# Kernel tuning notes

Hardware: AMD Instinct MI355X
Metric: run time of the kernel (lower is better)

Reference implementation:

```python
import jax, jax.numpy as jnp
import numpy as np

B, T, N, C_IN, C_OUT, CHEB_K, ST_EMB = 8, 12, 2048, 64, 64, 2, 64


def setup_inputs() -> dict:
    key = jax.random.key(0)
    ks = jax.random.split(key, 9)
    inv = 1.0 / np.sqrt(ST_EMB)
    return {
        "x": jax.random.normal(ks[0], (B, T, N, C_IN), dtype=jnp.float32),
        "adj": jax.random.uniform(ks[1], (N, N), dtype=jnp.float32),
        "st_emb": jax.random.normal(ks[2], (T, 1, ST_EMB), dtype=jnp.float32),
        "weights": jax.random.normal(ks[3], (CHEB_K, C_IN, C_OUT), dtype=jnp.float32) * 0.02,
        "bias": jax.random.normal(ks[4], (C_OUT,), dtype=jnp.float32) * 0.02,
        "W1": jax.random.uniform(ks[5], (ST_EMB, 32), minval=-inv, maxval=inv, dtype=jnp.float32),
        "b1": jax.random.uniform(ks[6], (32,), minval=-inv, maxval=inv, dtype=jnp.float32),
        "W2": jax.random.uniform(ks[7], (32, 1), minval=-1/np.sqrt(32), maxval=1/np.sqrt(32), dtype=jnp.float32),
        "b2": jax.random.uniform(ks[8], (1,), minval=-1/np.sqrt(32), maxval=1/np.sqrt(32), dtype=jnp.float32),
    }


def reference(x, adj, st_emb, weights, bias, W1, b1, W2, b2):
    # lambda MLP: Linear -> ReLU -> Linear, then 1 + relu(.)
    h = jax.nn.relu(st_emb @ W1 + b1)            # [T,1,32]
    lam = 1.0 + jax.nn.relu(h @ W2 + b2)         # [T,1,1]
    c1 = (2.0 * lam - 2.0) / lam                 # [T,1,1] diagonal-scale coefficient
    c2 = 2.0 / lam                               # [T,1,1]
    # identity support einsum == per-time diagonal scaling of x
    x_g1 = c1[None] * x                          # [B,T,N,C]
    # adjacency support: scale factored out of the N x N contraction
    x_g2 = c2[None] * jnp.einsum('nm,btmc->btnc', adj, x)  # [B,T,N,C]
    x_g = jnp.stack([x_g1, x_g2], axis=3)        # [B,T,N,K,C]
    return jnp.einsum('btnki,kio->btno', x_g, weights) + bias
```

## Files before the change

### kernel.cpp

```cpp
#include <hip/hip_runtime.h>
#include <hip/hip_bf16.h>

#define B_ 8
#define T_ 12
#define N_ 2048
#define C_ 64
#define BM 128
#define BK 64

typedef __attribute__((ext_vector_type(4))) float f32x4;
typedef __attribute__((ext_vector_type(4))) __bf16 bf16x4;
typedef __attribute__((ext_vector_type(8))) __bf16 bf16x8;

#define GAS __attribute__((address_space(1)))
#define LAS __attribute__((address_space(3)))

static __device__ __forceinline__ void gld_lds16(const void* g, void* l) {
    __builtin_amdgcn_global_load_lds((const GAS void*)g, (LAS void*)l, 16, 0, 0);
}

#define WS_CBUF 0
#define WS_WTB  1024
#define WS_ADJB 32768
#define WS_P1T  (32768 + 8388608)
#define WS_P0S  (WS_P1T + 25165824)
#define WS_MID  ((size_t)WS_P0S)
#define WS_FULL ((size_t)WS_P0S + 25165824)

__global__ void lam_kernel(const float* __restrict__ st, const float* __restrict__ W1,
                           const float* __restrict__ b1, const float* __restrict__ W2,
                           const float* __restrict__ b2, float* __restrict__ cbuf) {
    const int t = threadIdx.x >> 5;
    const int h = threadIdx.x & 31;
    if (t >= T_) return;
    float acc = b1[h];
    #pragma unroll 8
    for (int e = 0; e < 64; ++e) acc += st[t * 64 + e] * W1[e * 32 + h];
    float hv = fmaxf(acc, 0.f) * W2[h];
    #pragma unroll
    for (int off = 16; off; off >>= 1) hv += __shfl_down(hv, off, 32);
    if (h == 0) {
        float lam = 1.f + fmaxf(hv + b2[0], 0.f);
        cbuf[t]      = 2.f - 2.f / lam;
        cbuf[T_ + t] = 2.f / lam;
    }
}

__global__ void lamw_kernel(const float* __restrict__ st, const float* __restrict__ W1,
                            const float* __restrict__ b1, const float* __restrict__ W2,
                            const float* __restrict__ b2, const float* __restrict__ weights,
                            float* __restrict__ cbuf, __bf16* __restrict__ WtB) {
    const int t = threadIdx.x >> 5;
    const int h = threadIdx.x & 31;
    if (t < T_) {
        float acc = b1[h];
        #pragma unroll 8
        for (int e = 0; e < 64; ++e) acc += st[t * 64 + e] * W1[e * 32 + h];
        float hv = fmaxf(acc, 0.f) * W2[h];
        #pragma unroll
        for (int off = 16; off; off >>= 1) hv += __shfl_down(hv, off, 32);
        if (h == 0) {
            float lam = 1.f + fmaxf(hv + b2[0], 0.f);
            cbuf[t]      = 2.f - 2.f / lam;
            cbuf[T_ + t] = 2.f / lam;
        }
    }
    for (int e = threadIdx.x; e < 64 * 128; e += 512) {
        int o = e >> 7, k = e & 127;
        float v = (k < 64) ? weights[4096 + k * 64 + o] : weights[(k - 64) * 64 + o];
        WtB[o * 128 + k] = (__bf16)v;
    }
}

template<bool FULLP>
__global__ __launch_bounds__(256, 4) void pcvt_kernel(
    const float* __restrict__ x, const float* __restrict__ adj,
    const __bf16* __restrict__ WtB, const float* __restrict__ cbuf,
    const float* __restrict__ bias, __bf16* __restrict__ adjb,
    __bf16* __restrict__ P1T, __bf16* __restrict__ P0S, float* __restrict__ out)
{
    const int bid = blockIdx.x;
    const int tid = threadIdx.x;
    if (bid >= 1536) {
        const size_t i = ((size_t)(bid - 1536) * 256 + tid) * 8;
        const float4 f0 = *(const float4*)&adj[i];
        const float4 f1 = *(const float4*)&adj[i + 4];
        bf16x8 h = { (__bf16)f0.x, (__bf16)f0.y, (__bf16)f0.z, (__bf16)f0.w,
                     (__bf16)f1.x, (__bf16)f1.y, (__bf16)f1.z, (__bf16)f1.w };
        *(bf16x8*)&adjb[i] = h;
        return;
    }
    __shared__ __align__(16) __bf16 T[64 * 128];
    char* TB = (char*)T;
    const int bt = bid >> 4, n0 = (bid & 15) * 128;
    const int l = tid & 63, w = tid >> 6;
    const int lr = l & 15, lk = l >> 4;
    const float c1 = cbuf[bt % T_];

    f32x4 p1[2][4] = {}, p0[2][4] = {};
    #pragma unroll
    for (int ks = 0; ks < 2; ++ks) {
        bf16x8 a[2];
        #pragma unroll
        for (int mi = 0; mi < 2; ++mi) {
            const float* xs = x + ((size_t)bt * N_ + n0 + w * 32 + mi * 16 + lr) * C_ + ks * 32 + lk * 8;
            float4 f0 = *(const float4*)xs;
            float4 f1 = *(const float4*)(xs + 4);
            a[mi] = { (__bf16)f0.x, (__bf16)f0.y, (__bf16)f0.z, (__bf16)f0.w,
                      (__bf16)f1.x, (__bf16)f1.y, (__bf16)f1.z, (__bf16)f1.w };
        }
        #pragma unroll
        for (int nj = 0; nj < 4; ++nj) {
            const __bf16* wb = WtB + (nj * 16 + lr) * 128 + ks * 32 + lk * 8;
            bf16x8 b1v = *(const bf16x8*)wb;
            bf16x8 b0v = *(const bf16x8*)(wb + 64);
            #pragma unroll
            for (int mi = 0; mi < 2; ++mi) {
                p1[mi][nj] = __builtin_amdgcn_mfma_f32_16x16x32_bf16(a[mi], b1v, p1[mi][nj], 0, 0, 0);
                p0[mi][nj] = __builtin_amdgcn_mfma_f32_16x16x32_bf16(a[mi], b0v, p0[mi][nj], 0, 0, 0);
            }
        }
    }
    #pragma unroll
    for (int nj = 0; nj < 4; ++nj) {
        const int o = nj * 16 + lr;
        const float bv = bias[o];
        #pragma unroll
        for (int mi = 0; mi < 2; ++mi)
            #pragma unroll
            for (int q = 0; q < 4; ++q) {
                const int row = w * 32 + mi * 16 + lk * 4 + q;
                const size_t idx = ((size_t)bt * N_ + n0 + row) * C_ + o;
                const float v = c1 * p0[mi][nj][q] + bv;
                if (FULLP) P0S[idx] = (__bf16)v; else out[idx] = v;
            }
    }
    #pragma unroll
    for (int nj = 0; nj < 4; ++nj) {
        const int o = nj * 16 + lr;
        #pragma unroll
        for (int mi = 0; mi < 2; ++mi)
            #pragma unroll
            for (int q = 0; q < 4; ++q) {
                const int row = w * 32 + mi * 16 + lk * 4 + q;
                *(__bf16*)(TB + o * 256 + ((row * 2) ^ ((o & 7) << 4))) = (__bf16)p1[mi][nj][q];
            }
    }
    __syncthreads();
    {
        const int o = tid >> 2, seg = tid & 3;
        __bf16* dst = P1T + ((size_t)bt * 64 + o) * N_ + n0 + seg * 32;
        #pragma unroll
        for (int i = 0; i < 4; ++i) {
            const int chunk = seg * 64 + i * 16;
            *(bf16x8*)(dst + i * 8) = *(const bf16x8*)(TB + o * 256 + (chunk ^ ((o & 7) << 4)));
        }
    }
}

template<bool FULLP>
__global__ __launch_bounds__(256, 2) void dgcn_main3(
    const __bf16* __restrict__ adjb, const __bf16* __restrict__ P1T,
    const __bf16* __restrict__ P0S, const float* __restrict__ cbuf,
    float* __restrict__ out)
{
    __shared__ __align__(16) __bf16 smem[40960];
    char* sb = (char*)smem;

    const int m0  = blockIdx.x * BM;
    const int btg = blockIdx.y;
    const int tid = threadIdx.x;
    const int l   = tid & 63, w = tid >> 6;
    const int wr  = w >> 1, wc = w & 1;
    const int lr  = l & 15, lk = l >> 4;

    const __bf16* srcA[4];
    const __bf16* srcB[6];
    #pragma unroll
    for (int i = 0; i < 4; ++i) {
        int s = (w * 4 + i) * 64 + l;
        int r = s >> 3, j = s & 7;
        srcA[i] = adjb + (size_t)(m0 + r) * N_ + 8 * (j ^ (r & 7));
    }
    #pragma unroll
    for (int i = 0; i < 6; ++i) {
        int s = (w * 6 + i) * 64 + l;
        int btl = s >> 9, rem = s & 511;
        int o = rem >> 3, j = rem & 7;
        srcB[i] = P1T + ((size_t)(btg * 3 + btl) * 64 + o) * N_ + 8 * (j ^ (o & 7));
    }

    f32x4 acc[4][6] = {};

    #pragma unroll
    for (int i = 0; i < 4; ++i) gld_lds16(srcA[i], sb + (w * 4 + i) * 1024);
    #pragma unroll
    for (int i = 0; i < 6; ++i) gld_lds16(srcB[i], sb + 16384 + (w * 6 + i) * 1024);

    int sel = 0;
    for (int kt = 0; kt < N_ / BK; ++kt) {
        __syncthreads();
        if (kt < N_ / BK - 1) {
            const int wo = (sel ^ 1) * 40960;
            #pragma unroll
            for (int i = 0; i < 4; ++i) {
                srcA[i] += BK;
                gld_lds16(srcA[i], sb + wo + (w * 4 + i) * 1024);
            }
            #pragma unroll
            for (int i = 0; i < 6; ++i) {
                srcB[i] += BK;
                gld_lds16(srcB[i], sb + wo + 16384 + (w * 6 + i) * 1024);
            }
        }
        const char* base = sb + sel * 40960;
        #pragma unroll
        for (int ks = 0; ks < 2; ++ks) {
            const int kb = ks * 64 + lk * 16;
            bf16x8 a[4];
            #pragma unroll
            for (int mi = 0; mi < 4; ++mi) {
                int rr = wr * 64 + mi * 16 + lr;
                a[mi] = *(const bf16x8*)(base + rr * 128 + (kb ^ ((rr & 7) << 4)));
            }
            #pragma unroll
            for (int nj = 0; nj < 6; ++nj) {
                int c = wc * 96 + nj * 16 + lr;
                int btl = c >> 6, o = c & 63;
                bf16x8 b = *(const bf16x8*)(base + 16384 + btl * 8192 + o * 128 + (kb ^ ((o & 7) << 4)));
                #pragma unroll
                for (int mi = 0; mi < 4; ++mi)
                    acc[mi][nj] = __builtin_amdgcn_mfma_f32_16x16x32_bf16(a[mi], b, acc[mi][nj], 0, 0, 0);
            }
        }
        sel ^= 1;
    }

    #pragma unroll
    for (int nj = 0; nj < 6; ++nj) {
        const int c = wc * 96 + nj * 16 + lr;
        const int btl = c >> 6, o = c & 63;
        const int btA = btg * 3 + btl;
        const float c2 = cbuf[T_ + (btA % T_)];
        #pragma unroll
        for (int mi = 0; mi < 4; ++mi)
            #pragma unroll
            for (int q = 0; q < 4; ++q) {
                const int row = wr * 64 + mi * 16 + lk * 4 + q;
                const size_t idx = ((size_t)btA * N_ + m0 + row) * C_ + o;
                const float p0v = FULLP ? (float)P0S[idx] : out[idx];
                out[idx] = c2 * acc[mi][nj][q] + p0v;
            }
    }
}

#define LDM 72
#define LDE 136
__global__ __launch_bounds__(256, 3) void dgcn_fb(
    const float* __restrict__ x, const float* __restrict__ adj,
    const float* __restrict__ weights, const float* __restrict__ bias,
    const float* __restrict__ cbuf, float* __restrict__ out)
{
    __shared__ __align__(16) __bf16 smem[BM * LDE];
    __shared__ __align__(16) __bf16 Wt[64 * LDE];
    __bf16* As = smem;
    __bf16* Bs = smem + BM * LDM;
    __bf16* E  = smem;

    const int mtile = blockIdx.x;
    const int bt    = blockIdx.y;
    const int tloc  = bt % T_;
    const int m0    = mtile * BM;
    const int tid   = threadIdx.x;
    const int lane  = tid & 63;
    const int w     = tid >> 6;

    const float c1 = cbuf[tloc];
    const float c2 = cbuf[T_ + tloc];
    const float* xbt = x + (size_t)bt * N_ * C_;

    for (int e = tid; e < 2 * 64 * 64; e += 256) {
        int kk = e >> 6, o = e & 63;
        float v = (kk < 64) ? weights[4096 + kk * 64 + o] : weights[(kk - 64) * 64 + o];
        Wt[o * LDE + kk] = (__bf16)v;
    }

    f32x4 acc[2][4] = {};
    const int c4 = tid & 15;
    const int rg = tid >> 4;
    const int lr = lane & 15;
    const int lk = lane >> 4;

    for (int kt = 0; kt < N_ / BK; ++kt) {
        const int k0 = kt * BK;
        __syncthreads();
        #pragma unroll
        for (int j = 0; j < 8; ++j) {
            const int r = rg + 16 * j;
            const float4 f = *(const float4*)&adj[(size_t)(m0 + r) * N_ + k0 + 4 * c4];
            bf16x4 h = { (__bf16)f.x, (__bf16)f.y, (__bf16)f.z, (__bf16)f.w };
            *(bf16x4*)&As[r * LDM + 4 * c4] = h;
        }
        #pragma unroll
        for (int j = 0; j < 4; ++j) {
            const int k  = (tid & 15) + 16 * j;
            const int c0 = 4 * (tid >> 4);
            const float4 f = *(const float4*)&xbt[(size_t)(k0 + k) * C_ + c0];
            Bs[(c0 + 0) * LDM + k] = (__bf16)f.x;
            Bs[(c0 + 1) * LDM + k] = (__bf16)f.y;
            Bs[(c0 + 2) * LDM + k] = (__bf16)f.z;
            Bs[(c0 + 3) * LDM + k] = (__bf16)f.w;
        }
        __syncthreads();
        #pragma unroll
        for (int ks = 0; ks < 2; ++ks) {
            bf16x8 a0 = *(const bf16x8*)&As[(w * 32 +  0 + lr) * LDM + ks * 32 + lk * 8];
            bf16x8 a1 = *(const bf16x8*)&As[(w * 32 + 16 + lr) * LDM + ks * 32 + lk * 8];
            #pragma unroll
            for (int nj = 0; nj < 4; ++nj) {
                bf16x8 b = *(const bf16x8*)&Bs[(nj * 16 + lr) * LDM + ks * 32 + lk * 8];
                acc[0][nj] = __builtin_amdgcn_mfma_f32_16x16x32_bf16(a0, b, acc[0][nj], 0, 0, 0);
                acc[1][nj] = __builtin_amdgcn_mfma_f32_16x16x32_bf16(a1, b, acc[1][nj], 0, 0, 0);
            }
        }
    }
    __syncthreads();

    #pragma unroll
    for (int j = 0; j < 8; ++j) {
        const int r = rg + 16 * j;
        const float4 f = *(const float4*)&xbt[(size_t)(m0 + r) * C_ + 4 * c4];
        bf16x4 h = { (__bf16)(c1 * f.x), (__bf16)(c1 * f.y), (__bf16)(c1 * f.z), (__bf16)(c1 * f.w) };
        *(bf16x4*)&E[r * LDE + 64 + 4 * c4] = h;
    }
    #pragma unroll
    for (int mi = 0; mi < 2; ++mi)
        #pragma unroll
        for (int nj = 0; nj < 4; ++nj)
            #pragma unroll
            for (int q = 0; q < 4; ++q) {
                const int row = w * 32 + mi * 16 + lk * 4 + q;
                const int col = nj * 16 + lr;
                E[row * LDE + col] = (__bf16)(c2 * acc[mi][nj][q]);
            }
    __syncthreads();

    f32x4 oacc[2][4] = {};
    #pragma unroll
    for (int ks = 0; ks < 4; ++ks) {
        bf16x8 a0 = *(const bf16x8*)&E[(w * 32 +  0 + lr) * LDE + ks * 32 + lk * 8];
        bf16x8 a1 = *(const bf16x8*)&E[(w * 32 + 16 + lr) * LDE + ks * 32 + lk * 8];
        #pragma unroll
        for (int nj = 0; nj < 4; ++nj) {
            bf16x8 bw = *(const bf16x8*)&Wt[(nj * 16 + lr) * LDE + ks * 32 + lk * 8];
            oacc[0][nj] = __builtin_amdgcn_mfma_f32_16x16x32_bf16(a0, bw, oacc[0][nj], 0, 0, 0);
            oacc[1][nj] = __builtin_amdgcn_mfma_f32_16x16x32_bf16(a1, bw, oacc[1][nj], 0, 0, 0);
        }
    }
    float* obt = out + (size_t)bt * N_ * C_;
    #pragma unroll
    for (int nj = 0; nj < 4; ++nj) {
        const float bv = bias[nj * 16 + lr];
        #pragma unroll
        for (int mi = 0; mi < 2; ++mi)
            #pragma unroll
            for (int q = 0; q < 4; ++q) {
                const int row = w * 32 + mi * 16 + lk * 4 + q;
                obt[(size_t)(m0 + row) * C_ + nj * 16 + lr] = oacc[mi][nj][q] + bv;
            }
    }
}

extern "C" void kernel_launch(void* const* d_in, const int* in_sizes, int n_in,
                              void* d_out, int out_size, void* d_ws, size_t ws_size,
                              hipStream_t stream) {
    const float* x       = (const float*)d_in[0];
    const float* adj     = (const float*)d_in[1];
    const float* st_emb  = (const float*)d_in[2];
    const float* weights = (const float*)d_in[3];
    const float* bias    = (const float*)d_in[4];
    const float* W1      = (const float*)d_in[5];
    const float* b1      = (const float*)d_in[6];
    const float* W2      = (const float*)d_in[7];
    const float* b2      = (const float*)d_in[8];
    float* out = (float*)d_out;
    char* ws = (char*)d_ws;
    float* cbuf = (float*)(ws + WS_CBUF);

    if (ws_size >= WS_MID) {
        __bf16* WtB  = (__bf16*)(ws + WS_WTB);
        __bf16* adjb = (__bf16*)(ws + WS_ADJB);
        __bf16* P1T  = (__bf16*)(ws + WS_P1T);
        __bf16* P0S  = (__bf16*)(ws + WS_P0S);
        lamw_kernel<<<1, 512, 0, stream>>>(st_emb, W1, b1, W2, b2, weights, cbuf, WtB);
        if (ws_size >= WS_FULL) {
            pcvt_kernel<true><<<3584, 256, 0, stream>>>(x, adj, WtB, cbuf, bias, adjb, P1T, P0S, out);
            dgcn_main3<true><<<dim3(N_ / BM, 32), 256, 0, stream>>>(adjb, P1T, P0S, cbuf, out);
        } else {
            pcvt_kernel<false><<<3584, 256, 0, stream>>>(x, adj, WtB, cbuf, bias, adjb, P1T, P0S, out);
            dgcn_main3<false><<<dim3(N_ / BM, 32), 256, 0, stream>>>(adjb, P1T, P0S, cbuf, out);
        }
    } else {
        lam_kernel<<<1, 384, 0, stream>>>(st_emb, W1, b1, W2, b2, cbuf);
        dgcn_fb<<<dim3(N_ / BM, B_ * T_), 256, 0, stream>>>(x, adj, weights, bias, cbuf, out);
    }
}
```

Before: 95.58 us.

## Shrink main GEMM tile to two bt slices and single-buffer LDS

The main adjacency GEMM kernel now covers two batch-time slices per block (128 columns) instead of three, which doubles grid.y from 32 to 48. Software double buffering is replaced by a single LDS buffer with load, sync, compute. LDS use and per-thread accumulators shrink, and launch bounds ask for three blocks per CU to raise occupancy. In exchange, loads are no longer overlapped with MFMA work inside a block, and adjacency tiles are re-read more often because each block reuses them across fewer columns.

```diff
diff --git a/kernel.cpp b/kernel.cpp
--- a/kernel.cpp
+++ b/kernel.cpp
@@ -159,12 +159,12 @@
 }
 
 template<bool FULLP>
-__global__ __launch_bounds__(256, 2) void dgcn_main3(
+__global__ __launch_bounds__(256, 3) void dgcn_main7(
     const __bf16* __restrict__ adjb, const __bf16* __restrict__ P1T,
     const __bf16* __restrict__ P0S, const float* __restrict__ cbuf,
     float* __restrict__ out)
 {
-    __shared__ __align__(16) __bf16 smem[40960];
+    __shared__ __align__(16) __bf16 smem[16384];
     char* sb = (char*)smem;
 
     const int m0  = blockIdx.x * BM;
@@ -175,45 +175,28 @@
     const int lr  = l & 15, lk = l >> 4;
 
     const __bf16* srcA[4];
-    const __bf16* srcB[6];
+    const __bf16* srcB[4];
     #pragma unroll
     for (int i = 0; i < 4; ++i) {
         int s = (w * 4 + i) * 64 + l;
         int r = s >> 3, j = s & 7;
         srcA[i] = adjb + (size_t)(m0 + r) * N_ + 8 * (j ^ (r & 7));
-    }
-    #pragma unroll
-    for (int i = 0; i < 6; ++i) {
-        int s = (w * 6 + i) * 64 + l;
-        int btl = s >> 9, rem = s & 511;
-        int o = rem >> 3, j = rem & 7;
-        srcB[i] = P1T + ((size_t)(btg * 3 + btl) * 64 + o) * N_ + 8 * (j ^ (o & 7));
-    }
-
-    f32x4 acc[4][6] = {};
-
-    #pragma unroll
-    for (int i = 0; i < 4; ++i) gld_lds16(srcA[i], sb + (w * 4 + i) * 1024);
-    #pragma unroll
-    for (int i = 0; i < 6; ++i) gld_lds16(srcB[i], sb + 16384 + (w * 6 + i) * 1024);
-
-    int sel = 0;
+        int bb = s >> 9, o = (s >> 3) & 63;
+        srcB[i] = P1T + ((size_t)(btg * 2 + bb) * 64 + o) * N_ + 8 * (j ^ (o & 7));
+    }
+
+    f32x4 acc[4][4] = {};
+
     for (int kt = 0; kt < N_ / BK; ++kt) {
         __syncthreads();
-        if (kt < N_ / BK - 1) {
-            const int wo = (sel ^ 1) * 40960;
-            #pragma unroll
-            for (int i = 0; i < 4; ++i) {
-                srcA[i] += BK;
-                gld_lds16(srcA[i], sb + wo + (w * 4 + i) * 1024);
-            }
-            #pragma unroll
-            for (int i = 0; i < 6; ++i) {
-                srcB[i] += BK;
-                gld_lds16(srcB[i], sb + wo + 16384 + (w * 6 + i) * 1024);
-            }
-        }
-        const char* base = sb + sel * 40960;
+        #pragma unroll
+        for (int i = 0; i < 4; ++i) {
+            gld_lds16(srcA[i], sb + (w * 4 + i) * 1024);
+            gld_lds16(srcB[i], sb + 16384 + (w * 4 + i) * 1024);
+            srcA[i] += BK;
+            srcB[i] += BK;
+        }
+        __syncthreads();
         #pragma unroll
         for (int ks = 0; ks < 2; ++ks) {
             const int kb = ks * 64 + lk * 16;
@@ -221,27 +204,24 @@
             #pragma unroll
             for (int mi = 0; mi < 4; ++mi) {
                 int rr = wr * 64 + mi * 16 + lr;
-                a[mi] = *(const bf16x8*)(base + rr * 128 + (kb ^ ((rr & 7) << 4)));
-            }
-            #pragma unroll
-            for (int nj = 0; nj < 6; ++nj) {
-                int c = wc * 96 + nj * 16 + lr;
-                int btl = c >> 6, o = c & 63;
-                bf16x8 b = *(const bf16x8*)(base + 16384 + btl * 8192 + o * 128 + (kb ^ ((o & 7) << 4)));
+                a[mi] = *(const bf16x8*)(sb + rr * 128 + (kb ^ ((rr & 7) << 4)));
+            }
+            #pragma unroll
+            for (int nj = 0; nj < 4; ++nj) {
+                int cc = nj * 16 + lr;
+                bf16x8 b = *(const bf16x8*)(sb + 16384 + wc * 8192 + cc * 128 + (kb ^ ((cc & 7) << 4)));
                 #pragma unroll
                 for (int mi = 0; mi < 4; ++mi)
                     acc[mi][nj] = __builtin_amdgcn_mfma_f32_16x16x32_bf16(a[mi], b, acc[mi][nj], 0, 0, 0);
             }
         }
-        sel ^= 1;
-    }
-
-    #pragma unroll
-    for (int nj = 0; nj < 6; ++nj) {
-        const int c = wc * 96 + nj * 16 + lr;
-        const int btl = c >> 6, o = c & 63;
-        const int btA = btg * 3 + btl;
-        const float c2 = cbuf[T_ + (btA % T_)];
+    }
+
+    const int btA = btg * 2 + wc;
+    const float c2 = cbuf[T_ + (btA % T_)];
+    #pragma unroll
+    for (int nj = 0; nj < 4; ++nj) {
+        const int o = nj * 16 + lr;
         #pragma unroll
         for (int mi = 0; mi < 4; ++mi)
             #pragma unroll
@@ -395,10 +375,10 @@
         lamw_kernel<<<1, 512, 0, stream>>>(st_emb, W1, b1, W2, b2, weights, cbuf, WtB);
         if (ws_size >= WS_FULL) {
             pcvt_kernel<true><<<3584, 256, 0, stream>>>(x, adj, WtB, cbuf, bias, adjb, P1T, P0S, out);
-            dgcn_main3<true><<<dim3(N_ / BM, 32), 256, 0, stream>>>(adjb, P1T, P0S, cbuf, out);
+            dgcn_main7<true><<<dim3(N_ / BM, B_ * T_ / 2), 256, 0, stream>>>(adjb, P1T, P0S, cbuf, out);
         } else {
             pcvt_kernel<false><<<3584, 256, 0, stream>>>(x, adj, WtB, cbuf, bias, adjb, P1T, P0S, out);
-            dgcn_main3<false><<<dim3(N_ / BM, 32), 256, 0, stream>>>(adjb, P1T, P0S, cbuf, out);
+            dgcn_main7<false><<<dim3(N_ / BM, B_ * T_ / 2), 256, 0, stream>>>(adjb, P1T, P0S, cbuf, out);
         }
     } else {
         lam_kernel<<<1, 384, 0, stream>>>(st_emb, W1, b1, W2, b2, cbuf);
```

After: 99.17 us. +3.8%, slower.
